# Performance work log

Hardware: AMD Instinct MI355X
Metric: run time of the kernel (lower is better)

## Reference

```python
import jax, jax.numpy as jnp
import numpy as np

H = 8          # head_num
NEG = -1e9     # mask fill value
LN_EPS = 1e-6


def setup_inputs() -> dict:
    key = jax.random.key(0)
    ks = jax.random.split(key, 12)
    B, S, D = 8, 1024, 512
    inp = {
        'q': jax.random.normal(ks[0], (B, S, D), jnp.float32),
        'k': jax.random.normal(ks[1], (B, S, D), jnp.float32),
        'v': jax.random.normal(ks[2], (B, S, D), jnp.float32),
        'query_mask': jax.random.randint(ks[3], (B, S), 0, 2, jnp.int32),
        'key_mask': jax.random.randint(ks[4], (B, S), 0, 2, jnp.int32),
        'Wq': jax.random.normal(ks[5], (D, D), jnp.float32) / np.sqrt(D),
        'bq': jax.random.normal(ks[6], (D,), jnp.float32) * 0.02,
        'Wk': jax.random.normal(ks[7], (D, D), jnp.float32) / np.sqrt(D),
        'bk': jax.random.normal(ks[8], (D,), jnp.float32) * 0.02,
        'Wv': jax.random.normal(ks[9], (D, D), jnp.float32) / np.sqrt(D),
        'bv': jax.random.normal(ks[10], (D,), jnp.float32) * 0.02,
        'gamma': jnp.ones((D,), jnp.float32),
        'beta': jnp.zeros((D,), jnp.float32),
    }
    return inp


def _to_batches(x):
    # [B,S,D] -> [B*H, S, D/H]  (batch-major head layout, as in torch code)
    B, S, D = x.shape
    return x.reshape(B, S, H, D // H).transpose(0, 2, 1, 3).reshape(B * H, S, D // H)


def _from_batches(x):
    BH, S, d = x.shape
    B = BH // H
    return x.reshape(B, H, S, d).transpose(0, 2, 1, 3).reshape(B, S, H * d)


def reference(q, k, v, query_mask, key_mask, Wq, bq, Wk, bk, Wv, bv, gamma, beta):
    # QKV linears + ReLU activation (activation=F.relu in original)
    _q = jax.nn.relu(q @ Wq.T + bq)
    _k = jax.nn.relu(k @ Wk.T + bk)
    _v = jax.nn.relu(v @ Wv.T + bv)
    _q, _k, _v = _to_batches(_q), _to_batches(_k), _to_batches(_v)  # [B*H,S,d]

    # masks tiled head-MAJOR (repeat(head_num,1) semantics): index = h*B + b
    km = jnp.tile(key_mask, (H, 1))[:, None, :]    # [B*H, 1, S_k]
    qm = jnp.tile(query_mask, (H, 1))[:, :, None]  # [B*H, S_q, 1]

    d = _q.shape[-1]
    scores = jnp.einsum('bqd,bkd->bqk', _q, _k) / jnp.sqrt(jnp.float32(d))
    scores = jnp.where(km == 0, NEG, scores)
    attn = jax.nn.softmax(scores, axis=-1)
    attn = attn * qm.astype(attn.dtype)            # multiplicative query mask
    # dropout: eval mode (rate applied only in training) -> identity
    y = jnp.einsum('bqk,bkd->bqd', attn, _v)
    y = _from_batches(y) + q                       # residual
    # LayerNorm over last dim
    mu = jnp.mean(y, axis=-1, keepdims=True)
    var = jnp.mean((y - mu) ** 2, axis=-1, keepdims=True)
    return gamma * (y - mu) / jnp.sqrt(var + LN_EPS) + beta
```

## Files before the change

### kernel.cpp

```cpp
#include <hip/hip_runtime.h>
#include <hip/hip_bf16.h>
#include <stdint.h>

constexpr int kB = 8, kH = 8, kS = 1024, kD = 512, kDH = 64;
constexpr float kNeg = -1e9f;
constexpr float kScaleLog2e = 0.125f * 1.4426950408889634f;

typedef __attribute__((ext_vector_type(8))) short bf16x8;
typedef __attribute__((ext_vector_type(4))) float f32x4;
typedef __attribute__((ext_vector_type(4))) unsigned short u16x4;

__device__ __forceinline__ unsigned short f2bf(float f) {
  union { float f; unsigned int u; } a; a.f = f;
  return (unsigned short)((a.u + 0x7FFFu + ((a.u >> 16) & 1u)) >> 16);
}

__device__ __forceinline__ unsigned int pk2bf(float lo, float hi) {
  union { __hip_bfloat162 h; unsigned int u; } cv;
  cv.h = __float22bfloat162_rn(make_float2(lo, hi));
  return cv.u;
}

__device__ __forceinline__ uint4 gload16(const void* p) {
  uint4 r;
  asm volatile("global_load_dwordx4 %0, %1, off" : "=v"(r) : "v"(p));
  return r;
}
__device__ __forceinline__ int gload4(const void* p) {
  int r;
  asm volatile("global_load_dword %0, %1, off" : "=v"(r) : "v"(p));
  return r;
}
#define WAIT_VMCNT(N) do { \
  asm volatile("s_waitcnt vmcnt(" #N ")" ::: "memory"); \
  __builtin_amdgcn_sched_barrier(0); } while (0)

__device__ __forceinline__ uint4 cvt4(uint4 a, uint4 b) {
  uint4 r;
  r.x = pk2bf(__uint_as_float(a.x), __uint_as_float(a.y));
  r.y = pk2bf(__uint_as_float(a.z), __uint_as_float(a.w));
  r.z = pk2bf(__uint_as_float(b.x), __uint_as_float(b.y));
  r.w = pk2bf(__uint_as_float(b.z), __uint_as_float(b.w));
  return r;
}

#if __has_builtin(__builtin_amdgcn_exp2f)
#define EXP2F(x) __builtin_amdgcn_exp2f(x)
#else
#define EXP2F(x) exp2f(x)
#endif

__global__ __launch_bounds__(256)
void wcvt_kernel(const float* __restrict__ wq, const float* __restrict__ wk,
                 const float* __restrict__ wv, unsigned short* __restrict__ wout)
{
  const int tid = blockIdx.x * 256 + threadIdx.x;
  const int z = tid >> 16;
  const int i = (tid & 65535) * 4;
  const float* W = (z == 0) ? wq : (z == 1) ? wk : wv;
  float4 v4 = *(const float4*)(W + i);
  u16x4 pk;
  pk[0] = f2bf(v4.x); pk[1] = f2bf(v4.y); pk[2] = f2bf(v4.z); pk[3] = f2bf(v4.w);
  *(u16x4*)(wout + (size_t)z * 262144 + i) = pk;
}

__global__ __launch_bounds__(256)
void qkv_gemm_kernel(const float* __restrict__ xq, const float* __restrict__ xk,
                     const float* __restrict__ xv,
                     const unsigned short* __restrict__ wbf,
                     const float* __restrict__ bq, const float* __restrict__ bk,
                     const float* __restrict__ bv,
                     unsigned short* __restrict__ wsout)
{
  __shared__ __align__(16) unsigned short As[2][128][72];
  __shared__ __align__(16) unsigned short Bs[2][128][72];

  const int bid = blockIdx.x;
  const int xcd = bid & 7;
  const int j = bid >> 3;
  const int x = j & 3;
  const int g = (j >> 2) * 8 + xcd;
  const int z = g >> 6;
  const int y = g & 63;

  const float* X    = (z == 0) ? xq : (z == 1) ? xk : xv;
  const unsigned short* Wb = wbf + (size_t)z * 262144;
  const float* bias = (z == 0) ? bq : (z == 1) ? bk : bv;
  unsigned short* out = wsout + (size_t)z * (kB * kS * kD);

  const int m0 = y * 128;
  const int n0 = x * 128;
  const int t = threadIdx.x;
  const int lane = t & 63;
  const int w = t >> 6;
  const int wr = w >> 1, wc = w & 1;
  const int l16 = lane & 15, lg = lane >> 4;

  const int row = t >> 3, c8 = (t & 7) * 8;
  const float* Xr = X + (size_t)(m0 + row) * kD + c8;
  const unsigned short* Wr = Wb + (size_t)(n0 + row) * kD + c8;

  f32x4 acc[4][4] = {};
  uint4 pa0, pa1, pa2, pa3, pa4, pa5, pa6, pa7, pb0, pb1, pb2, pb3;
  uint4 qa0, qa1, qa2, qa3, qa4, qa5, qa6, qa7, qb0, qb1, qb2, qb3;

  auto issueP = [&](int kt) {
    pa0 = gload16(Xr + kt);            pa1 = gload16(Xr + kt + 4);
    pa2 = gload16(Xr + 32 * kD + kt);  pa3 = gload16(Xr + 32 * kD + kt + 4);
    pa4 = gload16(Xr + 64 * kD + kt);  pa5 = gload16(Xr + 64 * kD + kt + 4);
    pa6 = gload16(Xr + 96 * kD + kt);  pa7 = gload16(Xr + 96 * kD + kt + 4);
    pb0 = gload16(Wr + kt);            pb1 = gload16(Wr + 32 * kD + kt);
    pb2 = gload16(Wr + 64 * kD + kt);  pb3 = gload16(Wr + 96 * kD + kt);
  };
  auto issueQ = [&](int kt) {
    qa0 = gload16(Xr + kt);            qa1 = gload16(Xr + kt + 4);
    qa2 = gload16(Xr + 32 * kD + kt);  qa3 = gload16(Xr + 32 * kD + kt + 4);
    qa4 = gload16(Xr + 64 * kD + kt);  qa5 = gload16(Xr + 64 * kD + kt + 4);
    qa6 = gload16(Xr + 96 * kD + kt);  qa7 = gload16(Xr + 96 * kD + kt + 4);
    qb0 = gload16(Wr + kt);            qb1 = gload16(Wr + 32 * kD + kt);
    qb2 = gload16(Wr + 64 * kD + kt);  qb3 = gload16(Wr + 96 * kD + kt);
  };
  auto writeP = [&]() {
    *(uint4*)&As[0][row][c8]      = cvt4(pa0, pa1);
    *(uint4*)&As[0][row + 32][c8] = cvt4(pa2, pa3);
    *(uint4*)&As[0][row + 64][c8] = cvt4(pa4, pa5);
    *(uint4*)&As[0][row + 96][c8] = cvt4(pa6, pa7);
    *(uint4*)&Bs[0][row][c8]      = pb0;
    *(uint4*)&Bs[0][row + 32][c8] = pb1;
    *(uint4*)&Bs[0][row + 64][c8] = pb2;
    *(uint4*)&Bs[0][row + 96][c8] = pb3;
  };
  auto writeQ = [&]() {
    *(uint4*)&As[1][row][c8]      = cvt4(qa0, qa1);
    *(uint4*)&As[1][row + 32][c8] = cvt4(qa2, qa3);
    *(uint4*)&As[1][row + 64][c8] = cvt4(qa4, qa5);
    *(uint4*)&As[1][row + 96][c8] = cvt4(qa6, qa7);
    *(uint4*)&Bs[1][row][c8]      = qb0;
    *(uint4*)&Bs[1][row + 32][c8] = qb1;
    *(uint4*)&Bs[1][row + 64][c8] = qb2;
    *(uint4*)&Bs[1][row + 96][c8] = qb3;
  };
  auto mfma_phase = [&](int buf) {
#pragma unroll
    for (int kk = 0; kk < 2; ++kk) {
      bf16x8 av[4], bv[4];
#pragma unroll
      for (int mf = 0; mf < 4; ++mf)
        av[mf] = *(const bf16x8*)&As[buf][wr * 64 + mf * 16 + l16][kk * 32 + lg * 8];
#pragma unroll
      for (int nf = 0; nf < 4; ++nf)
        bv[nf] = *(const bf16x8*)&Bs[buf][wc * 64 + nf * 16 + l16][kk * 32 + lg * 8];
#pragma unroll
      for (int nf = 0; nf < 4; ++nf)
#pragma unroll
        for (int mf = 0; mf < 4; ++mf)
          acc[mf][nf] = __builtin_amdgcn_mfma_f32_16x16x32_bf16(bv[nf], av[mf], acc[mf][nf], 0, 0, 0);
    }
  };

  issueP(0);
  issueQ(64);
#pragma unroll
  for (int i = 0; i < 6; i += 2) {
    WAIT_VMCNT(12);
    writeP();
    issueP((i + 2) * 64);
    __syncthreads();
    mfma_phase(0);
    WAIT_VMCNT(12);
    writeQ();
    issueQ((i + 3) * 64);
    __syncthreads();
    mfma_phase(1);
  }
  WAIT_VMCNT(12);
  writeP();
  __syncthreads();
  mfma_phase(0);
  WAIT_VMCNT(0);
  writeQ();
  __syncthreads();
  mfma_phase(1);

  if (z == 2) {
    const int mmbase = m0 + wr * 64;
    const int b_ = mmbase >> 10, sbase = mmbase & 1023;
#pragma unroll
    for (int nf = 0; nf < 4; ++nf) {
#pragma unroll
      for (int r = 0; r < 4; ++r) {
        const int n = n0 + wc * 64 + nf * 16 + lg * 4 + r;
        const float bval = bias[n];
        const int h = n >> 6, dd = n & 63;
        u16x4 pk;
#pragma unroll
        for (int mf = 0; mf < 4; ++mf) {
          float vv = acc[mf][nf][r] + bval;
          vv = vv > 0.f ? vv : 0.f;
          pk[mf] = f2bf(vv);
        }
        *(u16x4*)&out[((size_t)((b_ * kH + h) * kDH + dd)) * kS + sbase + l16 * 4] = pk;
      }
    }
  } else {
#pragma unroll
    for (int mf = 0; mf < 4; ++mf) {
      const int mm = m0 + wr * 64 + mf * 16 + l16;
      const int b_ = mm >> 10, s = mm & 1023;
#pragma unroll
      for (int nf = 0; nf < 4; ++nf) {
        const int nbase = n0 + wc * 64 + nf * 16 + lg * 4;
        const int h = nbase >> 6, dd = nbase & 63;
        u16x4 pk;
#pragma unroll
        for (int r = 0; r < 4; ++r) {
          float vv = acc[mf][nf][r] + bias[nbase + r];
          vv = vv > 0.f ? vv : 0.f;
          pk[r] = f2bf(vv);
        }
        *(u16x4*)&out[((size_t)(b_ * kH + h) * kS + s) * kDH + dd] = pk;
      }
    }
  }
}

__global__ __launch_bounds__(256)
void attn_kernel(const unsigned short* __restrict__ ws,
                 const int* __restrict__ key_mask,
                 float* __restrict__ y)
{
  __shared__ __align__(16) unsigned short Ks[2][64][72];
  __shared__ __align__(16) unsigned short Vts[2][64][72];
  __shared__ __align__(16) unsigned short Ps[4][32][72];
  __shared__ float kmadd[2][64];

  const unsigned short* Qw = ws;
  const unsigned short* Kw = ws + (size_t)1 * kB * kS * kD;
  const unsigned short* Vw = ws + (size_t)2 * kB * kS * kD;

  const int bid = blockIdx.x;
  const int xcd = bid & 7;
  const int j = bid >> 3;
  const int qx = j & 7;
  const int bh = (j >> 3) * 8 + xcd;

  const int q0 = qx * 128;
  const int t = threadIdx.x;
  const int w = t >> 6, lane = t & 63;
  const int l16 = lane & 15, lg = lane >> 4;
  const int b_ = bh / kH, h = bh % kH;

  const unsigned short* Qb = Qw + ((size_t)bh * kS + q0) * kDH;
  const unsigned short* Kb = Kw + (size_t)bh * kS * kDH;
  const unsigned short* Vb = Vw + (size_t)bh * kDH * kS;
  const int* km = key_mask + (bh % kB) * kS;

  const int srow = t >> 3, sc8 = (t & 7) * 8;
  const unsigned short* KbR0 = Kb + (size_t)srow * kDH + sc8;
  const unsigned short* KbR1 = Kb + (size_t)(srow + 32) * kDH + sc8;
  const unsigned short* VbR0 = Vb + (size_t)srow * kS + sc8;
  const unsigned short* VbR1 = Vb + (size_t)(srow + 32) * kS + sc8;

  bf16x8 aq[2][2];
#pragma unroll
  for (int u = 0; u < 2; ++u)
#pragma unroll
    for (int kk = 0; kk < 2; ++kk)
      aq[u][kk] = *(const bf16x8*)(Qb + (size_t)(w * 32 + u * 16 + l16) * kDH + kk * 32 + lg * 8);

  bf16x8 vone;
#pragma unroll
  for (int jj = 0; jj < 8; ++jj) vone[jj] = (short)0x3F80;

  f32x4 o[2][4] = {};
  f32x4 lacc[2] = {};

  uint4 ka0, ka1, va0, va1; int kma;
  uint4 kb0, kb1, vb0, vb1; int kmb;

  auto issueA = [&](int kv0) {
    ka0 = gload16(KbR0 + (size_t)kv0 * kDH);
    ka1 = gload16(KbR1 + (size_t)kv0 * kDH);
    va0 = gload16(VbR0 + kv0);
    va1 = gload16(VbR1 + kv0);
    kma = gload4(km + kv0 + (t & 63));
  };
  auto issueB = [&](int kv0) {
    kb0 = gload16(KbR0 + (size_t)kv0 * kDH);
    kb1 = gload16(KbR1 + (size_t)kv0 * kDH);
    vb0 = gload16(VbR0 + kv0);
    vb1 = gload16(VbR1 + kv0);
    kmb = gload4(km + kv0 + (t & 63));
  };
  auto writeA = [&]() {
    *(uint4*)&Ks[0][srow][sc8]       = ka0;
    *(uint4*)&Ks[0][srow + 32][sc8]  = ka1;
    *(uint4*)&Vts[0][srow][sc8]      = va0;
    *(uint4*)&Vts[0][srow + 32][sc8] = va1;
    if (t < 64) kmadd[0][t] = kma ? 0.f : kNeg;
  };
  auto writeB = [&]() {
    *(uint4*)&Ks[1][srow][sc8]       = kb0;
    *(uint4*)&Ks[1][srow + 32][sc8]  = kb1;
    *(uint4*)&Vts[1][srow][sc8]      = vb0;
    *(uint4*)&Vts[1][srow + 32][sc8] = vb1;
    if (t < 64) kmadd[1][t] = kmb ? 0.f : kNeg;
  };
  auto compute = [&](int buf) {
    f32x4 sc[2][4] = {};
#pragma unroll
    for (int kk = 0; kk < 2; ++kk) {
#pragma unroll
      for (int nf = 0; nf < 4; ++nf) {
        bf16x8 bfr = *(const bf16x8*)&Ks[buf][nf * 16 + l16][kk * 32 + lg * 8];
#pragma unroll
        for (int u = 0; u < 2; ++u)
          sc[u][nf] = __builtin_amdgcn_mfma_f32_16x16x32_bf16(aq[u][kk], bfr, sc[u][nf], 0, 0, 0);
      }
    }
    float madd[4];
#pragma unroll
    for (int nf = 0; nf < 4; ++nf) madd[nf] = kmadd[buf][nf * 16 + l16];
#pragma unroll
    for (int u = 0; u < 2; ++u) {
#pragma unroll
      for (int r = 0; r < 4; ++r) {
        const float p0 = EXP2F(fmaf(sc[u][0][r], kScaleLog2e, madd[0]));
        const float p1 = EXP2F(fmaf(sc[u][1][r], kScaleLog2e, madd[1]));
        const float p2 = EXP2F(fmaf(sc[u][2][r], kScaleLog2e, madd[2]));
        const float p3 = EXP2F(fmaf(sc[u][3][r], kScaleLog2e, madd[3]));
        const int prow = u * 16 + lg * 4 + r;
        uint2 pw;
        pw.x = __builtin_amdgcn_perm(__float_as_uint(p1), __float_as_uint(p0), 0x07060302u);
        pw.y = __builtin_amdgcn_perm(__float_as_uint(p3), __float_as_uint(p2), 0x07060302u);
        *(uint2*)&Ps[w][prow][l16 * 4] = pw;
      }
    }
#pragma unroll
    for (int kk = 0; kk < 2; ++kk) {
      bf16x8 a0 = *(const bf16x8*)&Ps[w][l16][kk * 32 + lg * 8];
      bf16x8 a1 = *(const bf16x8*)&Ps[w][16 + l16][kk * 32 + lg * 8];
#pragma unroll
      for (int nd = 0; nd < 4; ++nd) {
        bf16x8 bfr = *(const bf16x8*)&Vts[buf][nd * 16 + l16][kk * 32 + lg * 8];
        o[0][nd] = __builtin_amdgcn_mfma_f32_16x16x32_bf16(a0, bfr, o[0][nd], 0, 0, 0);
        o[1][nd] = __builtin_amdgcn_mfma_f32_16x16x32_bf16(a1, bfr, o[1][nd], 0, 0, 0);
      }
      lacc[0] = __builtin_amdgcn_mfma_f32_16x16x32_bf16(a0, vone, lacc[0], 0, 0, 0);
      lacc[1] = __builtin_amdgcn_mfma_f32_16x16x32_bf16(a1, vone, lacc[1], 0, 0, 0);
    }
  };

  issueA(0);
  issueB(64);
  for (int i = 0; i < 14; i += 2) {
    WAIT_VMCNT(5);
    writeA();
    issueA((i + 2) * 64);
    __syncthreads();
    compute(0);
    WAIT_VMCNT(5);
    writeB();
    issueB((i + 3) * 64);
    __syncthreads();
    compute(1);
  }
  WAIT_VMCNT(5);
  writeA();
  __syncthreads();
  compute(0);
  WAIT_VMCNT(0);
  writeB();
  __syncthreads();
  compute(1);

#pragma unroll
  for (int u = 0; u < 2; ++u) {
    float rinv[4];
#pragma unroll
    for (int r = 0; r < 4; ++r) rinv[r] = 1.f / lacc[u][r];
#pragma unroll
    for (int nd = 0; nd < 4; ++nd) {
#pragma unroll
      for (int r = 0; r < 4; ++r) {
        const int srowq = q0 + w * 32 + u * 16 + lg * 4 + r;
        y[((size_t)b_ * kS + srowq) * kD + h * kDH + nd * 16 + l16] = o[u][nd][r] * rinv[r];
      }
    }
  }
}

__global__ __launch_bounds__(256)
void ln_kernel(const float* __restrict__ y, const float* __restrict__ q,
               const int* __restrict__ qmask,
               const float* __restrict__ gamma, const float* __restrict__ beta,
               float* __restrict__ out)
{
  const int w = threadIdx.x >> 6, lane = threadIdx.x & 63;
  const int row = blockIdx.x * 4 + w;
  const int b_ = row >> 10, s = row & 1023;
  const int d0 = lane * 8;
  const int h = d0 >> 6;

  const float* yp = y + (size_t)row * kD + d0;
  const float* qp = q + (size_t)row * kD + d0;
  const int qm = qmask[((b_ * kH + h) % kB) * kS + s];

  float4 y0 = *(const float4*)yp, y1 = *(const float4*)(yp + 4);
  float4 q0 = *(const float4*)qp, q1 = *(const float4*)(qp + 4);
  float vals[8] = { y0.x, y0.y, y0.z, y0.w, y1.x, y1.y, y1.z, y1.w };
  float qs[8]   = { q0.x, q0.y, q0.z, q0.w, q1.x, q1.y, q1.z, q1.w };

  float sum = 0.f, ss = 0.f;
#pragma unroll
  for (int j = 0; j < 8; ++j) {
    const float val = (qm ? vals[j] : 0.f) + qs[j];
    vals[j] = val; sum += val; ss += val * val;
  }
#pragma unroll
  for (int off = 1; off < 64; off <<= 1) {
    sum += __shfl_xor(sum, off);
    ss  += __shfl_xor(ss, off);
  }
  const float mu = sum * (1.f / kD);
  const float var = ss * (1.f / kD) - mu * mu;
  const float rstd = rsqrtf(var + 1e-6f);

  float4 g0 = *(const float4*)(gamma + d0), g1 = *(const float4*)(gamma + d0 + 4);
  float4 be0 = *(const float4*)(beta + d0), be1 = *(const float4*)(beta + d0 + 4);
  float gs[8] = { g0.x, g0.y, g0.z, g0.w, g1.x, g1.y, g1.z, g1.w };
  float bs[8] = { be0.x, be0.y, be0.z, be0.w, be1.x, be1.y, be1.z, be1.w };

  float4 o0, o1;
  o0.x = gs[0] * (vals[0] - mu) * rstd + bs[0];
  o0.y = gs[1] * (vals[1] - mu) * rstd + bs[1];
  o0.z = gs[2] * (vals[2] - mu) * rstd + bs[2];
  o0.w = gs[3] * (vals[3] - mu) * rstd + bs[3];
  o1.x = gs[4] * (vals[4] - mu) * rstd + bs[4];
  o1.y = gs[5] * (vals[5] - mu) * rstd + bs[5];
  o1.z = gs[6] * (vals[6] - mu) * rstd + bs[6];
  o1.w = gs[7] * (vals[7] - mu) * rstd + bs[7];
  *(float4*)(out + (size_t)row * kD + d0) = o0;
  *(float4*)(out + (size_t)row * kD + d0 + 4) = o1;
}

extern "C" void kernel_launch(void* const* d_in, const int* in_sizes, int n_in,
                              void* d_out, int out_size, void* d_ws, size_t ws_size,
                              hipStream_t stream) {
  const float* q  = (const float*)d_in[0];
  const float* k  = (const float*)d_in[1];
  const float* v  = (const float*)d_in[2];
  const int* qmask = (const int*)d_in[3];
  const int* kmask = (const int*)d_in[4];
  const float* Wq = (const float*)d_in[5];
  const float* bq = (const float*)d_in[6];
  const float* Wk = (const float*)d_in[7];
  const float* bk = (const float*)d_in[8];
  const float* Wv = (const float*)d_in[9];
  const float* bv = (const float*)d_in[10];
  const float* gamma = (const float*)d_in[11];
  const float* beta  = (const float*)d_in[12];
  float* out = (float*)d_out;
  unsigned short* wsqkv = (unsigned short*)d_ws;
  unsigned short* wbf = (unsigned short*)d_out;

  wcvt_kernel<<<768, 256, 0, stream>>>(Wq, Wk, Wv, wbf);
  qkv_gemm_kernel<<<768, 256, 0, stream>>>(
      q, k, v, wbf, bq, bk, bv, wsqkv);
  attn_kernel<<<512, 256, 0, stream>>>(wsqkv, kmask, out);
  ln_kernel<<<2048, 256, 0, stream>>>(out, q, qmask, gamma, beta, out);
}
```

Baseline: 72.37 us.

## Widen QKV GEMM tile to 128x256 with single-buffered LDS

The QKV projection GEMM tile grows from 128x128 to 128x256 outputs per block, halving the grid to 384 blocks so each fp32 activation row is loaded and converted half as often. The two-stage LDS double buffer is replaced with a single LDS buffer, with register prefetch of the next k-slice and a full vmcnt(0) wait each iteration. The larger tile doubles the accumulator registers, which may lower occupancy, and the simpler pipeline adds a barrier per step and exposes more load latency. 384 blocks may also underfill the device's CUs.

```diff
diff --git a/kernel.cpp b/kernel.cpp
--- a/kernel.cpp
+++ b/kernel.cpp
@@ -72,16 +72,16 @@
                      const float* __restrict__ bv,
                      unsigned short* __restrict__ wsout)
 {
-  __shared__ __align__(16) unsigned short As[2][128][72];
-  __shared__ __align__(16) unsigned short Bs[2][128][72];
+  __shared__ __align__(16) unsigned short As[128][72];
+  __shared__ __align__(16) unsigned short Bs[256][72];
 
   const int bid = blockIdx.x;
   const int xcd = bid & 7;
   const int j = bid >> 3;
-  const int x = j & 3;
-  const int g = (j >> 2) * 8 + xcd;
-  const int z = g >> 6;
-  const int y = g & 63;
+  const int x = j & 1;
+  const int gg = (j >> 1) * 8 + xcd;
+  const int z = gg >> 6;
+  const int y = gg & 63;
 
   const float* X    = (z == 0) ? xq : (z == 1) ? xk : xv;
   const unsigned short* Wb = wbf + (size_t)z * 262144;
@@ -89,7 +89,7 @@
   unsigned short* out = wsout + (size_t)z * (kB * kS * kD);
 
   const int m0 = y * 128;
-  const int n0 = x * 128;
+  const int n0 = x * 256;
   const int t = threadIdx.x;
   const int lane = t & 63;
   const int w = t >> 6;
@@ -100,96 +100,71 @@
   const float* Xr = X + (size_t)(m0 + row) * kD + c8;
   const unsigned short* Wr = Wb + (size_t)(n0 + row) * kD + c8;
 
-  f32x4 acc[4][4] = {};
-  uint4 pa0, pa1, pa2, pa3, pa4, pa5, pa6, pa7, pb0, pb1, pb2, pb3;
-  uint4 qa0, qa1, qa2, qa3, qa4, qa5, qa6, qa7, qb0, qb1, qb2, qb3;
-
-  auto issueP = [&](int kt) {
-    pa0 = gload16(Xr + kt);            pa1 = gload16(Xr + kt + 4);
-    pa2 = gload16(Xr + 32 * kD + kt);  pa3 = gload16(Xr + 32 * kD + kt + 4);
-    pa4 = gload16(Xr + 64 * kD + kt);  pa5 = gload16(Xr + 64 * kD + kt + 4);
-    pa6 = gload16(Xr + 96 * kD + kt);  pa7 = gload16(Xr + 96 * kD + kt + 4);
-    pb0 = gload16(Wr + kt);            pb1 = gload16(Wr + 32 * kD + kt);
-    pb2 = gload16(Wr + 64 * kD + kt);  pb3 = gload16(Wr + 96 * kD + kt);
-  };
-  auto issueQ = [&](int kt) {
-    qa0 = gload16(Xr + kt);            qa1 = gload16(Xr + kt + 4);
-    qa2 = gload16(Xr + 32 * kD + kt);  qa3 = gload16(Xr + 32 * kD + kt + 4);
-    qa4 = gload16(Xr + 64 * kD + kt);  qa5 = gload16(Xr + 64 * kD + kt + 4);
-    qa6 = gload16(Xr + 96 * kD + kt);  qa7 = gload16(Xr + 96 * kD + kt + 4);
-    qb0 = gload16(Wr + kt);            qb1 = gload16(Wr + 32 * kD + kt);
-    qb2 = gload16(Wr + 64 * kD + kt);  qb3 = gload16(Wr + 96 * kD + kt);
-  };
-  auto writeP = [&]() {
-    *(uint4*)&As[0][row][c8]      = cvt4(pa0, pa1);
-    *(uint4*)&As[0][row + 32][c8] = cvt4(pa2, pa3);
-    *(uint4*)&As[0][row + 64][c8] = cvt4(pa4, pa5);
-    *(uint4*)&As[0][row + 96][c8] = cvt4(pa6, pa7);
-    *(uint4*)&Bs[0][row][c8]      = pb0;
-    *(uint4*)&Bs[0][row + 32][c8] = pb1;
-    *(uint4*)&Bs[0][row + 64][c8] = pb2;
-    *(uint4*)&Bs[0][row + 96][c8] = pb3;
-  };
-  auto writeQ = [&]() {
-    *(uint4*)&As[1][row][c8]      = cvt4(qa0, qa1);
-    *(uint4*)&As[1][row + 32][c8] = cvt4(qa2, qa3);
-    *(uint4*)&As[1][row + 64][c8] = cvt4(qa4, qa5);
-    *(uint4*)&As[1][row + 96][c8] = cvt4(qa6, qa7);
-    *(uint4*)&Bs[1][row][c8]      = qb0;
-    *(uint4*)&Bs[1][row + 32][c8] = qb1;
-    *(uint4*)&Bs[1][row + 64][c8] = qb2;
-    *(uint4*)&Bs[1][row + 96][c8] = qb3;
-  };
-  auto mfma_phase = [&](int buf) {
+  f32x4 acc[4][8] = {};
+  uint4 pa0, pa1, pa2, pa3, pa4, pa5, pa6, pa7;
+  uint4 pb0, pb1, pb2, pb3, pb4, pb5, pb6, pb7;
+
+  auto issue = [&](int kt) {
+    pa0 = gload16(Xr + kt);             pa1 = gload16(Xr + kt + 4);
+    pa2 = gload16(Xr + 32 * kD + kt);   pa3 = gload16(Xr + 32 * kD + kt + 4);
+    pa4 = gload16(Xr + 64 * kD + kt);   pa5 = gload16(Xr + 64 * kD + kt + 4);
+    pa6 = gload16(Xr + 96 * kD + kt);   pa7 = gload16(Xr + 96 * kD + kt + 4);
+    pb0 = gload16(Wr + kt);             pb1 = gload16(Wr + 32 * kD + kt);
+    pb2 = gload16(Wr + 64 * kD + kt);   pb3 = gload16(Wr + 96 * kD + kt);
+    pb4 = gload16(Wr + 128 * kD + kt);  pb5 = gload16(Wr + 160 * kD + kt);
+    pb6 = gload16(Wr + 192 * kD + kt);  pb7 = gload16(Wr + 224 * kD + kt);
+  };
+  auto lds_write = [&]() {
+    *(uint4*)&As[row][c8]       = cvt4(pa0, pa1);
+    *(uint4*)&As[row + 32][c8]  = cvt4(pa2, pa3);
+    *(uint4*)&As[row + 64][c8]  = cvt4(pa4, pa5);
+    *(uint4*)&As[row + 96][c8]  = cvt4(pa6, pa7);
+    *(uint4*)&Bs[row][c8]       = pb0;
+    *(uint4*)&Bs[row + 32][c8]  = pb1;
+    *(uint4*)&Bs[row + 64][c8]  = pb2;
+    *(uint4*)&Bs[row + 96][c8]  = pb3;
+    *(uint4*)&Bs[row + 128][c8] = pb4;
+    *(uint4*)&Bs[row + 160][c8] = pb5;
+    *(uint4*)&Bs[row + 192][c8] = pb6;
+    *(uint4*)&Bs[row + 224][c8] = pb7;
+  };
+  auto mfma_phase = [&]() {
 #pragma unroll
     for (int kk = 0; kk < 2; ++kk) {
-      bf16x8 av[4], bv[4];
+      bf16x8 av[4], bv[8];
 #pragma unroll
       for (int mf = 0; mf < 4; ++mf)
-        av[mf] = *(const bf16x8*)&As[buf][wr * 64 + mf * 16 + l16][kk * 32 + lg * 8];
-#pragma unroll
-      for (int nf = 0; nf < 4; ++nf)
-        bv[nf] = *(const bf16x8*)&Bs[buf][wc * 64 + nf * 16 + l16][kk * 32 + lg * 8];
-#pragma unroll
-      for (int nf = 0; nf < 4; ++nf)
+        av[mf] = *(const bf16x8*)&As[wr * 64 + mf * 16 + l16][kk * 32 + lg * 8];
+#pragma unroll
+      for (int nf = 0; nf < 8; ++nf)
+        bv[nf] = *(const bf16x8*)&Bs[wc * 128 + nf * 16 + l16][kk * 32 + lg * 8];
+#pragma unroll
+      for (int nf = 0; nf < 8; ++nf)
 #pragma unroll
         for (int mf = 0; mf < 4; ++mf)
           acc[mf][nf] = __builtin_amdgcn_mfma_f32_16x16x32_bf16(bv[nf], av[mf], acc[mf][nf], 0, 0, 0);
     }
   };
 
-  issueP(0);
-  issueQ(64);
-#pragma unroll
-  for (int i = 0; i < 6; i += 2) {
-    WAIT_VMCNT(12);
-    writeP();
-    issueP((i + 2) * 64);
+  issue(0);
+#pragma unroll
+  for (int i = 0; i < 8; ++i) {
+    if (i) __syncthreads();
+    WAIT_VMCNT(0);
+    lds_write();
+    if (i < 7) issue((i + 1) * 64);
     __syncthreads();
-    mfma_phase(0);
-    WAIT_VMCNT(12);
-    writeQ();
-    issueQ((i + 3) * 64);
-    __syncthreads();
-    mfma_phase(1);
-  }
-  WAIT_VMCNT(12);
-  writeP();
-  __syncthreads();
-  mfma_phase(0);
-  WAIT_VMCNT(0);
-  writeQ();
-  __syncthreads();
-  mfma_phase(1);
+    mfma_phase();
+  }
 
   if (z == 2) {
     const int mmbase = m0 + wr * 64;
     const int b_ = mmbase >> 10, sbase = mmbase & 1023;
 #pragma unroll
-    for (int nf = 0; nf < 4; ++nf) {
+    for (int nf = 0; nf < 8; ++nf) {
 #pragma unroll
       for (int r = 0; r < 4; ++r) {
-        const int n = n0 + wc * 64 + nf * 16 + lg * 4 + r;
+        const int n = n0 + wc * 128 + nf * 16 + lg * 4 + r;
         const float bval = bias[n];
         const int h = n >> 6, dd = n & 63;
         u16x4 pk;
@@ -208,8 +183,8 @@
       const int mm = m0 + wr * 64 + mf * 16 + l16;
       const int b_ = mm >> 10, s = mm & 1023;
 #pragma unroll
-      for (int nf = 0; nf < 4; ++nf) {
-        const int nbase = n0 + wc * 64 + nf * 16 + lg * 4;
+      for (int nf = 0; nf < 8; ++nf) {
+        const int nbase = n0 + wc * 128 + nf * 16 + lg * 4;
         const int h = nbase >> 6, dd = nbase & 63;
         u16x4 pk;
 #pragma unroll
@@ -465,7 +440,7 @@
   unsigned short* wbf = (unsigned short*)d_out;
 
   wcvt_kernel<<<768, 256, 0, stream>>>(Wq, Wk, Wv, wbf);
-  qkv_gemm_kernel<<<768, 256, 0, stream>>>(
+  qkv_gemm_kernel<<<384, 256, 0, stream>>>(
       q, k, v, wbf, bq, bk, bv, wsqkv);
   attn_kernel<<<512, 256, 0, stream>>>(wsqkv, kmask, out);
   ln_kernel<<<2048, 256, 0, stream>>>(out, q, qmask, gamma, beta, out);
```

Result: slower. 82.30 us (+13.7%).

## Pre-convert activations to bf16 and stream GEMM tiles via global-to-LDS loads

Applied to the files above, without the earlier changes.

Adds a combined conversion kernel that casts the q/k/v activations as well as the weights to bf16 in workspace. It then uses a new QKV GEMM that loads swizzled bf16 tiles straight into LDS with global_load_lds, rather than loading fp32 into registers and converting there. The aim is to halve the GEMM's activation read traffic and remove the in-register conversion and LDS store work. The cost is an extra full pass over the activations (fp32 read plus bf16 write) and a single-buffered LDS loop that waits on every tile with little load/compute overlap. The new path is chosen only when the workspace is at least 48 MiB; otherwise the old register-path GEMM runs.

```diff
diff --git a/kernel.cpp b/kernel.cpp
--- a/kernel.cpp
+++ b/kernel.cpp
@@ -14,13 +14,11 @@
   union { float f; unsigned int u; } a; a.f = f;
   return (unsigned short)((a.u + 0x7FFFu + ((a.u >> 16) & 1u)) >> 16);
 }
-
 __device__ __forceinline__ unsigned int pk2bf(float lo, float hi) {
   union { __hip_bfloat162 h; unsigned int u; } cv;
   cv.h = __float22bfloat162_rn(make_float2(lo, hi));
   return cv.u;
 }
-
 __device__ __forceinline__ uint4 gload16(const void* p) {
   uint4 r;
   asm volatile("global_load_dwordx4 %0, %1, off" : "=v"(r) : "v"(p));
@@ -43,6 +41,11 @@
   r.w = pk2bf(__uint_as_float(b.z), __uint_as_float(b.w));
   return r;
 }
+__device__ __forceinline__ void gll16(const unsigned short* g, unsigned short* l) {
+  __builtin_amdgcn_global_load_lds(
+      (const __attribute__((address_space(1))) unsigned int*)(g),
+      (__attribute__((address_space(3))) unsigned int*)(l), 16, 0, 0);
+}
 
 #if __has_builtin(__builtin_amdgcn_exp2f)
 #define EXP2F(x) __builtin_amdgcn_exp2f(x)
@@ -51,26 +54,161 @@
 #endif
 
 __global__ __launch_bounds__(256)
-void wcvt_kernel(const float* __restrict__ wq, const float* __restrict__ wk,
-                 const float* __restrict__ wv, unsigned short* __restrict__ wout)
+void cvt_all(const float* __restrict__ xq, const float* __restrict__ xk,
+             const float* __restrict__ xv,
+             const float* __restrict__ wq, const float* __restrict__ wk,
+             const float* __restrict__ wv,
+             unsigned short* __restrict__ xbf, unsigned short* __restrict__ wbf,
+             int do_x)
 {
-  const int tid = blockIdx.x * 256 + threadIdx.x;
-  const int z = tid >> 16;
-  const int i = (tid & 65535) * 4;
-  const float* W = (z == 0) ? wq : (z == 1) ? wk : wv;
-  float4 v4 = *(const float4*)(W + i);
-  u16x4 pk;
-  pk[0] = f2bf(v4.x); pk[1] = f2bf(v4.y); pk[2] = f2bf(v4.z); pk[3] = f2bf(v4.w);
-  *(u16x4*)(wout + (size_t)z * 262144 + i) = pk;
+  constexpr int kXElems = 3 * 4194304;
+  constexpr int kTotal  = kXElems + 3 * 262144;
+  for (int idx = blockIdx.x * 256 + threadIdx.x; idx * 4 < kTotal;
+       idx += gridDim.x * 256) {
+    const int i4 = idx * 4;
+    const float* src;
+    unsigned short* dst;
+    if (i4 < kXElems) {
+      if (!do_x) continue;
+      const int z = i4 >> 22, off = i4 & 4194303;
+      src = ((z == 0) ? xq : (z == 1) ? xk : xv) + off;
+      dst = xbf + (size_t)z * 4194304 + off;
+    } else {
+      const int j = i4 - kXElems;
+      const int z = j >> 18, off = j & 262143;
+      src = ((z == 0) ? wq : (z == 1) ? wk : wv) + off;
+      dst = wbf + (size_t)z * 262144 + off;
+    }
+    float4 v4 = *(const float4*)src;
+    u16x4 pk;
+    pk[0] = f2bf(v4.x); pk[1] = f2bf(v4.y); pk[2] = f2bf(v4.z); pk[3] = f2bf(v4.w);
+    *(u16x4*)dst = pk;
+  }
 }
 
 __global__ __launch_bounds__(256)
-void qkv_gemm_kernel(const float* __restrict__ xq, const float* __restrict__ xk,
-                     const float* __restrict__ xv,
-                     const unsigned short* __restrict__ wbf,
-                     const float* __restrict__ bq, const float* __restrict__ bk,
-                     const float* __restrict__ bv,
-                     unsigned short* __restrict__ wsout)
+void qkv_gemm_lds(const unsigned short* __restrict__ xbf,
+                  const unsigned short* __restrict__ wbf,
+                  const float* __restrict__ bq, const float* __restrict__ bk,
+                  const float* __restrict__ bv,
+                  unsigned short* __restrict__ wsout)
+{
+  __shared__ __align__(16) unsigned short As[128][64];
+  __shared__ __align__(16) unsigned short Bs[128][64];
+
+  const int bid = blockIdx.x;
+  const int xcd = bid & 7;
+  const int j = bid >> 3;
+  const int x = j & 3;
+  const int g = (j >> 2) * 8 + xcd;
+  const int z = g >> 6;
+  const int y = g & 63;
+
+  const unsigned short* Xb = xbf + (size_t)z * 4194304;
+  const unsigned short* Wb = wbf + (size_t)z * 262144;
+  const float* bias = (z == 0) ? bq : (z == 1) ? bk : bv;
+  unsigned short* out = wsout + (size_t)z * (kB * kS * kD);
+
+  const int m0 = y * 128;
+  const int n0 = x * 128;
+  const int t = threadIdx.x;
+  const int lane = t & 63;
+  const int w = t >> 6;
+  const int wr = w >> 1, wc = w & 1;
+  const int l16 = lane & 15, lg = lane >> 4;
+
+  f32x4 acc[4][4] = {};
+
+  auto issue = [&](int kt) {
+#pragma unroll
+    for (int i = 0; i < 4; ++i) {
+      const int s = w * 64 + lane + 256 * i;
+      const int r = s >> 3, c = s & 7;
+      const int cs = (c ^ (r & 7)) * 8;
+      unsigned short* ldsoff = (unsigned short*)&As[0][0] + (size_t)(w * 64 + 256 * i) * 8;
+      gll16(Xb + (size_t)(m0 + r) * kD + kt + cs, ldsoff);
+      unsigned short* ldsoffB = (unsigned short*)&Bs[0][0] + (size_t)(w * 64 + 256 * i) * 8;
+      gll16(Wb + (size_t)(n0 + r) * kD + kt + cs, ldsoffB);
+    }
+  };
+  auto mfma_phase = [&]() {
+#pragma unroll
+    for (int kk = 0; kk < 2; ++kk) {
+      const int x0 = ((kk * 4 + lg) ^ (l16 & 7)) * 8;
+      bf16x8 av[4], bv_[4];
+#pragma unroll
+      for (int mf = 0; mf < 4; ++mf)
+        av[mf] = *(const bf16x8*)&As[wr * 64 + mf * 16 + l16][x0];
+#pragma unroll
+      for (int nf = 0; nf < 4; ++nf)
+        bv_[nf] = *(const bf16x8*)&Bs[wc * 64 + nf * 16 + l16][x0];
+#pragma unroll
+      for (int nf = 0; nf < 4; ++nf)
+#pragma unroll
+        for (int mf = 0; mf < 4; ++mf)
+          acc[mf][nf] = __builtin_amdgcn_mfma_f32_16x16x32_bf16(bv_[nf], av[mf], acc[mf][nf], 0, 0, 0);
+    }
+  };
+
+  issue(0);
+#pragma unroll
+  for (int i = 0; i < 8; ++i) {
+    WAIT_VMCNT(0);
+    __syncthreads();
+    mfma_phase();
+    __syncthreads();
+    if (i < 7) issue((i + 1) * 64);
+  }
+
+  if (z == 2) {
+    const int mmbase = m0 + wr * 64;
+    const int b_ = mmbase >> 10, sbase = mmbase & 1023;
+#pragma unroll
+    for (int nf = 0; nf < 4; ++nf) {
+#pragma unroll
+      for (int r = 0; r < 4; ++r) {
+        const int n = n0 + wc * 64 + nf * 16 + lg * 4 + r;
+        const float bval = bias[n];
+        const int h = n >> 6, dd = n & 63;
+        u16x4 pk;
+#pragma unroll
+        for (int mf = 0; mf < 4; ++mf) {
+          float vv = acc[mf][nf][r] + bval;
+          vv = vv > 0.f ? vv : 0.f;
+          pk[mf] = f2bf(vv);
+        }
+        *(u16x4*)&out[((size_t)((b_ * kH + h) * kDH + dd)) * kS + sbase + l16 * 4] = pk;
+      }
+    }
+  } else {
+#pragma unroll
+    for (int mf = 0; mf < 4; ++mf) {
+      const int mm = m0 + wr * 64 + mf * 16 + l16;
+      const int b_ = mm >> 10, s = mm & 1023;
+#pragma unroll
+      for (int nf = 0; nf < 4; ++nf) {
+        const int nbase = n0 + wc * 64 + nf * 16 + lg * 4;
+        const int h = nbase >> 6, dd = nbase & 63;
+        u16x4 pk;
+#pragma unroll
+        for (int r = 0; r < 4; ++r) {
+          float vv = acc[mf][nf][r] + bias[nbase + r];
+          vv = vv > 0.f ? vv : 0.f;
+          pk[r] = f2bf(vv);
+        }
+        *(u16x4*)&out[((size_t)(b_ * kH + h) * kS + s) * kDH + dd] = pk;
+      }
+    }
+  }
+}
+
+__global__ __launch_bounds__(256)
+void qkv_gemm_reg(const float* __restrict__ xq, const float* __restrict__ xk,
+                  const float* __restrict__ xv,
+                  const unsigned short* __restrict__ wbf,
+                  const float* __restrict__ bq, const float* __restrict__ bk,
+                  const float* __restrict__ bv,
+                  unsigned short* __restrict__ wsout)
 {
   __shared__ __align__(16) unsigned short As[2][128][72];
   __shared__ __align__(16) unsigned short Bs[2][128][72];
@@ -462,11 +600,18 @@
   const float* beta  = (const float*)d_in[12];
   float* out = (float*)d_out;
   unsigned short* wsqkv = (unsigned short*)d_ws;
-  unsigned short* wbf = (unsigned short*)d_out;
-
-  wcvt_kernel<<<768, 256, 0, stream>>>(Wq, Wk, Wv, wbf);
-  qkv_gemm_kernel<<<768, 256, 0, stream>>>(
-      q, k, v, wbf, bq, bk, bv, wsqkv);
+  unsigned short* xbf   = wsqkv + (size_t)3 * 4194304;
+  unsigned short* wbf   = (unsigned short*)d_out;
+
+  const bool lds_path = ws_size >= (size_t)48 * 1024 * 1024;
+
+  cvt_all<<<1024, 256, 0, stream>>>(q, k, v, Wq, Wk, Wv, xbf, wbf,
+                                    lds_path ? 1 : 0);
+  if (lds_path) {
+    qkv_gemm_lds<<<768, 256, 0, stream>>>(xbf, wbf, bq, bk, bv, wsqkv);
+  } else {
+    qkv_gemm_reg<<<768, 256, 0, stream>>>(q, k, v, wbf, bq, bk, bv, wsqkv);
+  }
   attn_kernel<<<512, 256, 0, stream>>>(wsqkv, kmask, out);
   ln_kernel<<<2048, 256, 0, stream>>>(out, q, qmask, gamma, beta, out);
 }
```

After: 78.31 us. 8.2% more time.
